# Kernel tuning notes

Hardware: AMD Instinct MI355X
Metric: run time of the kernel (lower is better)

The kernel has to match this reference:

```python
import jax, jax.numpy as jnp
import numpy as np

N, D_IN, D, K = 8192, 1024, 256, 30
SCALE = D ** (-0.5)


def setup_inputs() -> dict:
    key = jax.random.key(0)
    ks = jax.random.split(key, 10)
    p = lambda k, sh: (jax.random.normal(k, sh, dtype=jnp.float32) * 0.02)
    return {
        'x_path': jax.random.normal(ks[0], (N, D_IN), dtype=jnp.float32),
        'W_fc1': p(ks[1], (D_IN, D)), 'b_fc1': jnp.zeros((D,), jnp.float32),
        'W_fc2': p(ks[2], (D, D)),   'b_fc2': jnp.zeros((D,), jnp.float32),
        'W_head': p(ks[3], (D, D)),  'b_head': jnp.zeros((D,), jnp.float32),
        'W_tail': p(ks[4], (D, D)),  'b_tail': jnp.zeros((D,), jnp.float32),
        'W_lin1': p(ks[5], (D, D)),  'b_lin1': jnp.zeros((D,), jnp.float32),
        'W_lin2': p(ks[6], (D, D)),  'b_lin2': jnp.zeros((D,), jnp.float32),
        'W_att1': p(ks[7], (D, D // 2)), 'b_att1': jnp.zeros((D // 2,), jnp.float32),
        'W_att2': p(ks[8], (D // 2, 1)), 'b_att2': jnp.zeros((1,), jnp.float32),
    }


def reference(x_path, W_fc1, b_fc1, W_fc2, b_fc2, W_head, b_head, W_tail, b_tail,
              W_lin1, b_lin1, W_lin2, b_lin2, W_att1, b_att1, W_att2, b_att2):
    # pathology_fc (eval mode, dropout = identity): 1024 -> 256 -> 256
    h = jax.nn.relu(x_path @ W_fc1 + b_fc1)
    h = jax.nn.relu(h @ W_fc2 + b_fc2)                      # [N, D]

    e_h = h @ W_head + b_head                               # [N, D]
    e_t = h @ W_tail + b_tail                               # [N, D]

    # pairwise scores + topk neighbor selection
    attn_logit = (e_h * SCALE) @ e_t.T                      # [N, N]
    topk_w, topk_i = jax.lax.top_k(attn_logit, K)           # [N, K]
    topk_prob = jax.nn.softmax(topk_w, axis=-1)             # [N, K]

    Nb_h = e_t[topk_i]                                      # gather neighbors [N, K, D]

    # gated message construction
    eh_r = topk_prob[..., None] * Nb_h + (1.0 - topk_prob)[..., None] * e_h[:, None, :]
    gate = jnp.tanh(e_h[:, None, :] + eh_r)                 # [N, K, D]

    # torch.einsum('ijkl,ijkm->ijk', Nb_h, gate): l and m summed independently
    ka_weight = Nb_h.sum(-1) * gate.sum(-1)                 # [N, K]
    ka_prob = jax.nn.softmax(ka_weight, axis=-1)            # [N, K]
    e_Nh = jnp.einsum('nk,nkd->nd', ka_prob, Nb_h)          # [N, D]

    sum_emb = jax.nn.relu((e_h + e_Nh) @ W_lin1 + b_lin1)
    bi_emb = jax.nn.relu((e_h * e_Nh) @ W_lin2 + b_lin2)
    e = sum_emb + bi_emb                                    # [N, D]

    # GlobalAttention readout
    att = jax.nn.leaky_relu(e @ W_att1 + b_att1, 0.01) @ W_att2 + b_att2   # [N, 1]
    a = jax.nn.softmax(att, axis=0)                         # softmax over nodes
    e_g = (a * e).sum(0)                                    # [D]
    return e, e_g
```

## Files before the change

kernel.cpp:

```cpp
#include <hip/hip_runtime.h>
#include <math.h>

#define NN   8192
#define DIN  1024
#define DD   256
#define TOPK 30
#define KP   40
#define CAP  88
#define NINF -3e38f

typedef short s8v  __attribute__((ext_vector_type(8)));
typedef float f16v __attribute__((ext_vector_type(16)));

__device__ __forceinline__ float wred_sum(float v) {
  v += __shfl_down(v, 32); v += __shfl_down(v, 16); v += __shfl_down(v, 8);
  v += __shfl_down(v, 4);  v += __shfl_down(v, 2);  v += __shfl_down(v, 1);
  return v;
}
__device__ __forceinline__ float wred_max(float v) {
  v = fmaxf(v, __shfl_down(v, 32)); v = fmaxf(v, __shfl_down(v, 16));
  v = fmaxf(v, __shfl_down(v, 8));  v = fmaxf(v, __shfl_down(v, 4));
  v = fmaxf(v, __shfl_down(v, 2));  v = fmaxf(v, __shfl_down(v, 1));
  return v;
}
__device__ __forceinline__ float tanh_fast(float x) {
  return 1.f - 2.f / (__expf(2.f * x) + 1.f);
}
__device__ __forceinline__ unsigned short f2bf(float x) {
  union { float f; unsigned int u; } v; v.f = x;
  unsigned int r = v.u + 0x7FFF + ((v.u >> 16) & 1);
  return (unsigned short)(r >> 16);
}
__device__ __forceinline__ bool pair_gt(float v, int i, float pv, int pi) {
  return (v > pv) || (v == pv && i < pi);
}
__device__ __forceinline__ unsigned key_pack(float f, int col) {
  unsigned b = __float_as_uint(f);
  unsigned u = ((int)b < 0) ? ~b : (b | 0x80000000u);
  return (u & 0xFFFFE000u) | (unsigned)col;
}

template<int ACT, int AOP, int ACCUM>
__global__ __launch_bounds__(128, 4)
void gemm_k(const float* __restrict__ A, const float* __restrict__ A2,
            const float* __restrict__ B, const float* __restrict__ bias,
            float* __restrict__ C, int K, int NB)
{
  __shared__ float sA[32 * 36];
  __shared__ float sB[32 * 68];
  const int t  = threadIdx.x;
  const int rb = blockIdx.x * 32;
  const int cb = blockIdx.y * 64;
  const int tr = t >> 4;
  const int tc = t & 15;

  float acc[4][4];
#pragma unroll
  for (int u = 0; u < 4; ++u)
#pragma unroll
    for (int j = 0; j < 4; ++j) acc[u][j] = 0.f;

  const int sr  = t >> 2;
  const int sk2 = (t & 3) * 4;

  for (int kt = 0; kt < K; kt += 32) {
    __syncthreads();
    {
      const float* Ap = A + (size_t)(rb + sr) * K + kt;
      float4 va = *(const float4*)(Ap + sk2);
      float4 vb = *(const float4*)(Ap + sk2 + 16);
      if (AOP) {
        const float* A2p = A2 + (size_t)(rb + sr) * K + kt;
        const float4 wa = *(const float4*)(A2p + sk2);
        const float4 wb = *(const float4*)(A2p + sk2 + 16);
        if (AOP == 1) {
          va.x += wa.x; va.y += wa.y; va.z += wa.z; va.w += wa.w;
          vb.x += wb.x; vb.y += wb.y; vb.z += wb.z; vb.w += wb.w;
        } else {
          va.x *= wa.x; va.y *= wa.y; va.z *= wa.z; va.w *= wa.w;
          vb.x *= wb.x; vb.y *= wb.y; vb.z *= wb.z; vb.w *= wb.w;
        }
      }
      sA[(sk2 + 0) * 36 + sr] = va.x; sA[(sk2 + 1) * 36 + sr] = va.y;
      sA[(sk2 + 2) * 36 + sr] = va.z; sA[(sk2 + 3) * 36 + sr] = va.w;
      sA[(sk2 + 16) * 36 + sr] = vb.x; sA[(sk2 + 17) * 36 + sr] = vb.y;
      sA[(sk2 + 18) * 36 + sr] = vb.z; sA[(sk2 + 19) * 36 + sr] = vb.w;
    }
    {
#pragma unroll
      for (int i = 0; i < 4; ++i) {
        const int f4 = t + 128 * i;
        const int k  = f4 >> 4;
        const int c4 = (f4 & 15) << 2;
        *(float4*)&sB[k * 68 + c4] = *(const float4*)&B[(size_t)(kt + k) * NB + cb + c4];
      }
    }
    __syncthreads();
#pragma unroll 8
    for (int k = 0; k < 32; ++k) {
      const float4 bv = *(const float4*)&sB[k * 68 + 4 * tc];
      const float4 av = *(const float4*)&sA[k * 36 + 4 * tr];
      const float a[4] = {av.x, av.y, av.z, av.w};
      const float b[4] = {bv.x, bv.y, bv.z, bv.w};
#pragma unroll
      for (int u = 0; u < 4; ++u)
#pragma unroll
        for (int j = 0; j < 4; ++j) acc[u][j] = fmaf(a[u], b[j], acc[u][j]);
    }
  }

  const float4 bz = *(const float4*)&bias[cb + 4 * tc];
  const float bb[4] = {bz.x, bz.y, bz.z, bz.w};
#pragma unroll
  for (int u = 0; u < 4; ++u) {
    const int row = rb + 4 * tr + u;
    float o[4];
#pragma unroll
    for (int j = 0; j < 4; ++j) {
      o[j] = acc[u][j] + bb[j];
      if (ACT) o[j] = fmaxf(o[j], 0.f);
    }
    float* Cp = &C[(size_t)row * NB + cb + 4 * tc];
    if (ACCUM) {
      const float4 old = *(const float4*)Cp;
      o[0] += old.x; o[1] += old.y; o[2] += old.z; o[3] += old.w;
    }
    float4 ov; ov.x = o[0]; ov.y = o[1]; ov.z = o[2]; ov.w = o[3];
    *(float4*)Cp = ov;
  }
}

__global__ __launch_bounds__(256)
void pack_frag_k(const float* __restrict__ src, unsigned short* __restrict__ dst)
{
  const int c = blockIdx.x * 256 + threadIdx.x;
  const int l = c & 63;
  const int W = (c >> 6) & 15;
  const int T = c >> 10;
  const int col = T * 32 + (l & 31);
  const int k0  = W * 16 + ((l >> 5) << 3);
  const float4 a = *(const float4*)&src[(size_t)col * DD + k0];
  const float4 b = *(const float4*)&src[(size_t)col * DD + k0 + 4];
  uint4 o;
  o.x = (unsigned)f2bf(a.x) | ((unsigned)f2bf(a.y) << 16);
  o.y = (unsigned)f2bf(a.z) | ((unsigned)f2bf(a.w) << 16);
  o.z = (unsigned)f2bf(b.x) | ((unsigned)f2bf(b.y) << 16);
  o.w = (unsigned)f2bf(b.z) | ((unsigned)f2bf(b.w) << 16);
  *(uint4*)&dst[(size_t)c * 8] = o;
}

__global__ __launch_bounds__(256)
void rowsum_k(const float* __restrict__ et, float* __restrict__ rs)
{
  const int t = threadIdx.x, lane = t & 63, w = t >> 6;
  const int n = blockIdx.x * 4 + w;
  const float4 v = *(const float4*)&et[(size_t)n * DD + lane * 4];
  float s = v.x + v.y + v.z + v.w;
  s = wred_sum(s);
  if (lane == 0) rs[n] = s;
}

__global__ __launch_bounds__(512, 4)
void score_cand_k(const unsigned short* __restrict__ ehF,
                  const unsigned short* __restrict__ etF,
                  unsigned* __restrict__ gCand)
{
  __shared__ unsigned sBuf[32 * CAP];
  __shared__ unsigned sK[32][KP];
  __shared__ unsigned sThrK[32];
  __shared__ int      sCnt[32];

  const int t = threadIdx.x, lane = t & 63, w = t >> 6;
  const int g  = blockIdx.x;
  const int sy = blockIdx.y;
  const int tile0 = sy * 128;
  const s8v* eh8 = (const s8v*)ehF;
  const s8v* et8 = (const s8v*)etF;

  s8v af[16];
#pragma unroll
  for (int W = 0; W < 16; ++W)
    af[W] = eh8[((size_t)g * 16 + W) * 64 + lane];

  for (int idx = t; idx < 32 * KP; idx += 512) ((unsigned*)sK)[idx] = 0u;
  if (t < 32) { sThrK[t] = 0u; sCnt[t] = 0; }
  __syncthreads();

  const int rq = 4 * (lane >> 5);
  const int colLane = lane & 31;

  int tb = 0;
  for (int rnd = 0; rnd < 7; ++rnd) {
    const int ntile = (rnd == 0) ? 2 : (2 << (rnd - 1));
    for (int p = w; p < ntile; p += 8) {
      const int T = tile0 + tb + p;
      const s8v* bp = et8 + (size_t)T * 1024 + lane;
      f16v c;
#pragma unroll
      for (int i = 0; i < 16; ++i) c[i] = 0.f;
      {
        s8v b[8];
#pragma unroll
        for (int q = 0; q < 8; ++q) b[q] = bp[q * 64];
#pragma unroll
        for (int q = 0; q < 8; ++q)
          c = __builtin_amdgcn_mfma_f32_32x32x16_bf16(af[q], b[q], c, 0, 0, 0);
#pragma unroll
        for (int q = 0; q < 8; ++q) b[q] = bp[(8 + q) * 64];
#pragma unroll
        for (int q = 0; q < 8; ++q)
          c = __builtin_amdgcn_mfma_f32_32x32x16_bf16(af[8 + q], b[q], c, 0, 0, 0);
      }
      const int col = T * 32 + colLane;
#pragma unroll
      for (int r = 0; r < 16; ++r) {
        const int row = (r & 3) + 8 * (r >> 2) + rq;
        const unsigned key = key_pack(c[r], col);
        if (key > sThrK[row]) {
          const int ix = atomicAdd(&sCnt[row], 1);
          if (ix < CAP) sBuf[row * CAP + ix] = key;
        }
      }
    }
    __syncthreads();

#pragma unroll 1
    for (int rp = 0; rp < 2; ++rp) {
      const int ra = 4 * w + 2 * rp;
      const int rc = ra + 1;
      const int cA = min(sCnt[ra], CAP);
      const int cB = min(sCnt[rc], CAP);
      unsigned a0 = (lane < KP) ? sK[ra][lane]
                                : ((lane - KP) < cA ? sBuf[ra * CAP + (lane - KP)] : 0u);
      unsigned a1 = ((24 + lane) < cA) ? sBuf[ra * CAP + 24 + lane] : 0u;
      unsigned b0 = (lane < KP) ? sK[rc][lane]
                                : ((lane - KP) < cB ? sBuf[rc * CAP + (lane - KP)] : 0u);
      unsigned b1 = ((24 + lane) < cB) ? sBuf[rc * CAP + 24 + lane] : 0u;
#pragma unroll
      for (int k = 2; k <= 128; k <<= 1) {
#pragma unroll
        for (int j = k >> 1; j >= 1; j >>= 1) {
          if (j == 64) {
            unsigned mx = max(a0, a1), mn = min(a0, a1); a0 = mx; a1 = mn;
            mx = max(b0, b1); mn = min(b0, b1); b0 = mx; b1 = mn;
          } else {
            const unsigned pa0 = (unsigned)__shfl_xor((int)a0, j);
            const unsigned pa1 = (unsigned)__shfl_xor((int)a1, j);
            const unsigned pb0 = (unsigned)__shfl_xor((int)b0, j);
            const unsigned pb1 = (unsigned)__shfl_xor((int)b1, j);
            const bool km0 = (((lane & k) == 0)        == ((lane & j) == 0));
            const bool km1 = ((((64 + lane) & k) == 0) == ((lane & j) == 0));
            a0 = km0 ? max(a0, pa0) : min(a0, pa0);
            a1 = km1 ? max(a1, pa1) : min(a1, pa1);
            b0 = km0 ? max(b0, pb0) : min(b0, pb0);
            b1 = km1 ? max(b1, pb1) : min(b1, pb1);
          }
        }
      }
      if (rnd < 6) {
        if (lane < KP) { sK[ra][lane] = a0; sK[rc][lane] = b0; }
        if (lane == KP - 1) { sThrK[ra] = a0; sThrK[rc] = b0; }
        if (lane == 0) { sCnt[ra] = 0; sCnt[rc] = 0; }
      } else {
        if (lane < KP) {
          gCand[(((size_t)g * 2 + sy) * 32 + ra) * KP + lane] = a0;
          gCand[(((size_t)g * 2 + sy) * 32 + rc) * KP + lane] = b0;
        }
      }
    }
    __syncthreads();
    tb += ntile;
  }
}

__global__ __launch_bounds__(512, 2)
void cand_merge_k(const unsigned* __restrict__ gCand,
                  const float* __restrict__ e_h, const float* __restrict__ e_t,
                  float* __restrict__ topv_g, int* __restrict__ topi_g)
{
  __shared__ float    sEh[32 * 256];
  __shared__ unsigned sK40[32][KP];
  __shared__ float    sRes[32][KP];
  const int t = threadIdx.x, lane = t & 63, w = t >> 6;
  const int g = blockIdx.x, rb = g * 32;

  for (int i = t; i < 2048; i += 512)
    ((float4*)sEh)[i] = ((const float4*)(e_h + (size_t)rb * 256))[i];

#pragma unroll 1
  for (int rr = 0; rr < 4; ++rr) {
    const int r = 4 * w + rr;
    unsigned v0, v1;
    {
      const int m = lane;
      const int s = m / 40, q = m - s * 40;
      v0 = gCand[(((size_t)g * 2 + s) * 32 + r) * KP + q];
    }
    {
      const int m = 64 + lane;
      if (m < 80) {
        const int q = m - 40;
        v1 = gCand[(((size_t)g * 2 + 1) * 32 + r) * KP + q];
      } else v1 = 0u;
    }
#pragma unroll
    for (int k = 2; k <= 128; k <<= 1) {
#pragma unroll
      for (int j = k >> 1; j >= 1; j >>= 1) {
        if (j == 64) {
          const unsigned mx = max(v0, v1), mn = min(v0, v1);
          v0 = mx; v1 = mn;
        } else {
          const unsigned p0 = (unsigned)__shfl_xor((int)v0, j);
          const unsigned p1 = (unsigned)__shfl_xor((int)v1, j);
          const bool km0 = (((lane & k) == 0)        == ((lane & j) == 0));
          const bool km1 = ((((64 + lane) & k) == 0) == ((lane & j) == 0));
          v0 = km0 ? max(v0, p0) : min(v0, p0);
          v1 = km1 ? max(v1, p1) : min(v1, p1);
        }
      }
    }
    if (lane < KP) sK40[r][lane] = v0;
  }
  __syncthreads();

  for (int i = t; i < 32 * KP; i += 512) {
    const int r = i / KP, q = i - r * KP;
    const int c = (int)(sK40[r][q] & 0x1FFFu);
    const float* et = &e_t[(size_t)c * 256];
    const float* eh = &sEh[r * 256];
    float acc = 0.f;
#pragma unroll 8
    for (int d = 0; d < 64; ++d) {
      const float4 a = *(const float4*)&eh[d * 4];
      const float4 b = *(const float4*)&et[d * 4];
      acc = fmaf(a.x, b.x, acc); acc = fmaf(a.y, b.y, acc);
      acc = fmaf(a.z, b.z, acc); acc = fmaf(a.w, b.w, acc);
    }
    sRes[r][q] = acc * 0.0625f;
  }
  __syncthreads();

#pragma unroll 1
  for (int rr = 0; rr < 4; ++rr) {
    const int r = 4 * w + rr;
    float v; int c;
    if (lane < KP) { v = sRes[r][lane]; c = (int)(sK40[r][lane] & 0x1FFFu); }
    else           { v = NINF;          c = 0x40000000 + lane; }
#pragma unroll
    for (int k = 2; k <= 64; k <<= 1) {
#pragma unroll
      for (int j = k >> 1; j >= 1; j >>= 1) {
        const float pv = __shfl_xor(v, j);
        const int   pc = __shfl_xor(c, j);
        const bool km = (((lane & k) == 0) == ((lane & j) == 0));
        const bool gt = pair_gt(v, c, pv, pc);
        const bool keep = (km == gt);
        v = keep ? v : pv; c = keep ? c : pc;
      }
    }
    if (lane < TOPK) {
      topv_g[(size_t)(rb + r) * TOPK + lane] = v;
      topi_g[(size_t)(rb + r) * TOPK + lane] = c;
    }
  }
}

__global__ __launch_bounds__(256)
void message_k(const float* __restrict__ e_h, const float* __restrict__ e_t,
               const float* __restrict__ rs, const float* __restrict__ tv_g,
               const int* __restrict__ ti_g, float* __restrict__ e_Nh)
{
  __shared__ float sP[TOPK];
  __shared__ int   sI[TOPK];
  __shared__ float sW[TOPK];
  __shared__ float wpart[TOPK][4];
  const int n = blockIdx.x;
  const int t = threadIdx.x, lane = t & 63, w = t >> 6;

  if (w == 0) {
    const float v = (lane < TOPK) ? tv_g[(size_t)n * TOPK + lane] : NINF;
    float m = wred_max(v); m = __shfl(m, 0);
    const float p = (lane < TOPK) ? __expf(v - m) : 0.f;
    float s = wred_sum(p); s = __shfl(s, 0);
    if (lane < TOPK) { sP[lane] = p / s; sI[lane] = ti_g[(size_t)n * TOPK + lane]; }
  }
  __syncthreads();

  const float eh = e_h[(size_t)n * DD + t];
  float nbv[TOPK];
#pragma unroll
  for (int k = 0; k < TOPK; ++k) {
    const int   j = sI[k];
    const float p = sP[k];
    const float nb = e_t[(size_t)j * DD + t];
    nbv[k] = nb;
    float g = tanh_fast((2.f - p) * eh + p * nb);
    g = wred_sum(g);
    if (lane == 0) wpart[k][w] = g;
  }
  __syncthreads();

  if (w == 0) {
    float kw = NINF;
    if (lane < TOPK) {
      const float gs = wpart[lane][0] + wpart[lane][1] + wpart[lane][2] + wpart[lane][3];
      kw = rs[sI[lane]] * gs;
    }
    float m = wred_max(kw); m = __shfl(m, 0);
    const float p = (lane < TOPK) ? __expf(kw - m) : 0.f;
    float s = wred_sum(p); s = __shfl(s, 0);
    if (lane < TOPK) sW[lane] = p / s;
  }
  __syncthreads();

  float o = 0.f;
#pragma unroll
  for (int k = 0; k < TOPK; ++k) o = fmaf(sW[k], nbv[k], o);
  e_Nh[(size_t)n * DD + t] = o;
}

__global__ __launch_bounds__(256)
void att_k(const float* __restrict__ e, const float* __restrict__ W1,
           const float* __restrict__ b1, const float* __restrict__ W2,
           const float* __restrict__ b2, float* __restrict__ att)
{
  const int t = threadIdx.x;
  const int q = t >> 7;
  const int m = t & 127;
  const int lane = t & 63, w = t >> 6;
  const int n0 = blockIdx.x * 8 + q * 4;
  float acc[4] = {0.f, 0.f, 0.f, 0.f};
  for (int d = 0; d < DD; ++d) {
    const float wv = W1[d * 128 + m];
#pragma unroll
    for (int rr = 0; rr < 4; ++rr)
      acc[rr] = fmaf(e[(size_t)(n0 + rr) * DD + d], wv, acc[rr]);
  }
  const float b1m = b1[m], w2m = W2[m];
  __shared__ float part[4][4];
#pragma unroll
  for (int rr = 0; rr < 4; ++rr) {
    float v = acc[rr] + b1m;
    v = (v > 0.f) ? v : 0.01f * v;
    v *= w2m;
    v = wred_sum(v);
    if (lane == 0) part[w][rr] = v;
  }
  __syncthreads();
  if (t < 8) {
    const int qq = t >> 2, rr = t & 3;
    att[blockIdx.x * 8 + qq * 4 + rr] = part[qq * 2][rr] + part[qq * 2 + 1][rr] + b2[0];
  }
}

__global__ __launch_bounds__(1024)
void smax_prep_k(const float* __restrict__ att, float* __restrict__ stats,
                 float* __restrict__ eg)
{
  __shared__ float red[16];
  __shared__ float mg;
  const int t = threadIdx.x, lane = t & 63, w = t >> 6;
  float m = NINF;
#pragma unroll
  for (int i = 0; i < 8; ++i) m = fmaxf(m, att[t + 1024 * i]);
  m = wred_max(m);
  if (lane == 0) red[w] = m;
  __syncthreads();
  if (t == 0) {
    float mm = red[0];
    for (int i = 1; i < 16; ++i) mm = fmaxf(mm, red[i]);
    mg = mm;
  }
  __syncthreads();
  const float mm = mg;
  float s = 0.f;
#pragma unroll
  for (int i = 0; i < 8; ++i) s += __expf(att[t + 1024 * i] - mm);
  s = wred_sum(s);
  __syncthreads();
  if (lane == 0) red[w] = s;
  __syncthreads();
  if (t == 0) {
    float ss = 0.f;
    for (int i = 0; i < 16; ++i) ss += red[i];
    stats[0] = mm; stats[1] = ss;
  }
  if (t < DD) eg[t] = 0.f;
}

__global__ __launch_bounds__(256)
void eg_k(const float* __restrict__ att, const float* __restrict__ stats,
          const float* __restrict__ e, float* __restrict__ eg)
{
  const int t = threadIdx.x;
  const float m = stats[0], inv = 1.f / stats[1];
  float acc = 0.f;
  const int n0 = blockIdx.x * 128;
  for (int r = 0; r < 128; ++r) {
    const int n = n0 + r;
    acc = fmaf(__expf(att[n] - m), e[(size_t)n * DD + t], acc);
  }
  atomicAdd(&eg[t], acc * inv);
}

extern "C" void kernel_launch(void* const* d_in, const int* in_sizes, int n_in,
                              void* d_out, int out_size, void* d_ws, size_t ws_size,
                              hipStream_t stream)
{
  const float* x      = (const float*)d_in[0];
  const float* W_fc1  = (const float*)d_in[1];
  const float* b_fc1  = (const float*)d_in[2];
  const float* W_fc2  = (const float*)d_in[3];
  const float* b_fc2  = (const float*)d_in[4];
  const float* W_head = (const float*)d_in[5];
  const float* b_head = (const float*)d_in[6];
  const float* W_tail = (const float*)d_in[7];
  const float* b_tail = (const float*)d_in[8];
  const float* W_lin1 = (const float*)d_in[9];
  const float* b_lin1 = (const float*)d_in[10];
  const float* W_lin2 = (const float*)d_in[11];
  const float* b_lin2 = (const float*)d_in[12];
  const float* W_att1 = (const float*)d_in[13];
  const float* b_att1 = (const float*)d_in[14];
  const float* W_att2 = (const float*)d_in[15];
  const float* b_att2 = (const float*)d_in[16];

  float* out_e  = (float*)d_out;
  float* out_eg = out_e + (size_t)NN * DD;

  float* ws = (float*)d_ws;
  const size_t F = (size_t)NN * DD;
  float* e_h   = ws;
  float* e_t   = ws + F;
  float* e_Nh  = ws + 2 * F;
  float* bufA  = ws + 3 * F;
  float* bufB  = ws + 4 * F;
  float* rs    = ws + 5 * F;
  float* att   = rs + NN;
  float* stats = att + NN;
  float* topv  = stats + 16;
  int*   topi  = (int*)(topv + (size_t)NN * TOPK);

  unsigned short* ehF = (unsigned short*)bufA;
  unsigned short* etF = ehF + F;
  unsigned* gCand = (unsigned*)bufB;

  const dim3 blk(256);
  const dim3 gblk(128);
  const dim3 gemmGrid(NN / 32, DD / 64);

  gemm_k<1,0,0><<<gemmGrid, gblk, 0, stream>>>(x,    nullptr, W_fc1, b_fc1, bufA, DIN, DD);
  gemm_k<1,0,0><<<gemmGrid, gblk, 0, stream>>>(bufA, nullptr, W_fc2, b_fc2, bufB, DD,  DD);
  gemm_k<0,0,0><<<gemmGrid, gblk, 0, stream>>>(bufB, nullptr, W_head, b_head, e_h, DD, DD);
  gemm_k<0,0,0><<<gemmGrid, gblk, 0, stream>>>(bufB, nullptr, W_tail, b_tail, e_t, DD, DD);

  pack_frag_k<<<dim3(NN * DD / 8 / 256), blk, 0, stream>>>(e_h, ehF);
  pack_frag_k<<<dim3(NN * DD / 8 / 256), blk, 0, stream>>>(e_t, etF);
  rowsum_k<<<dim3(NN / 4), blk, 0, stream>>>(e_t, rs);

  score_cand_k<<<dim3(NN / 32, 2), dim3(512), 0, stream>>>(ehF, etF, gCand);
  cand_merge_k<<<dim3(NN / 32), dim3(512), 0, stream>>>(gCand, e_h, e_t, topv, topi);

  message_k<<<dim3(NN), blk, 0, stream>>>(e_h, e_t, rs, topv, topi, e_Nh);

  gemm_k<1,1,0><<<gemmGrid, gblk, 0, stream>>>(e_h, e_Nh, W_lin1, b_lin1, out_e, DD, DD);
  gemm_k<1,2,1><<<gemmGrid, gblk, 0, stream>>>(e_h, e_Nh, W_lin2, b_lin2, out_e, DD, DD);

  att_k<<<dim3(NN / 8), blk, 0, stream>>>(out_e, W_att1, b_att1, W_att2, b_att2, att);
  smax_prep_k<<<dim3(1), dim3(1024), 0, stream>>>(att, stats, out_eg);
  eg_k<<<dim3(64), blk, 0, stream>>>(att, stats, out_e, out_eg);
}
```

Measured before the change: 666.1 us.

## Aggregate candidate atomics per half-wave, split MFMA chains, and halve merge blocks

In the score kernel, each row's candidate insertions now use a ballot and popcount so that one atomicAdd runs per half-wave instead of one per passing lane. Per-row thresholds are cached in registers once per round rather than read from shared memory for every element. The 16-MFMA dependency chain is split into two independent accumulators to shorten the serial latency. The merge kernel now handles 16 rows per block across a 2-wide grid, doubling block count for better occupancy, at the cost of two extra sums per score and duplicate candidate loads.

```diff
diff --git a/kernel.cpp b/kernel.cpp
--- a/kernel.cpp
+++ b/kernel.cpp
@@ -188,36 +188,48 @@
 
   const int rq = 4 * (lane >> 5);
   const int colLane = lane & 31;
+  const int leader = (lane >> 5) << 5;
+  const unsigned lm = (1u << (lane & 31)) - 1;
 
   int tb = 0;
   for (int rnd = 0; rnd < 7; ++rnd) {
     const int ntile = (rnd == 0) ? 2 : (2 << (rnd - 1));
+    unsigned thrv[16];
+#pragma unroll
+    for (int r = 0; r < 16; ++r) thrv[r] = sThrK[(r & 3) + 8 * (r >> 2) + rq];
+
     for (int p = w; p < ntile; p += 8) {
       const int T = tile0 + tb + p;
       const s8v* bp = et8 + (size_t)T * 1024 + lane;
-      f16v c;
-#pragma unroll
-      for (int i = 0; i < 16; ++i) c[i] = 0.f;
+      f16v c0, c1;
+#pragma unroll
+      for (int i = 0; i < 16; ++i) { c0[i] = 0.f; c1[i] = 0.f; }
       {
         s8v b[8];
 #pragma unroll
         for (int q = 0; q < 8; ++q) b[q] = bp[q * 64];
 #pragma unroll
         for (int q = 0; q < 8; ++q)
-          c = __builtin_amdgcn_mfma_f32_32x32x16_bf16(af[q], b[q], c, 0, 0, 0);
+          c0 = __builtin_amdgcn_mfma_f32_32x32x16_bf16(af[q], b[q], c0, 0, 0, 0);
 #pragma unroll
         for (int q = 0; q < 8; ++q) b[q] = bp[(8 + q) * 64];
 #pragma unroll
         for (int q = 0; q < 8; ++q)
-          c = __builtin_amdgcn_mfma_f32_32x32x16_bf16(af[8 + q], b[q], c, 0, 0, 0);
+          c1 = __builtin_amdgcn_mfma_f32_32x32x16_bf16(af[8 + q], b[q], c1, 0, 0, 0);
       }
       const int col = T * 32 + colLane;
 #pragma unroll
       for (int r = 0; r < 16; ++r) {
         const int row = (r & 3) + 8 * (r >> 2) + rq;
-        const unsigned key = key_pack(c[r], col);
-        if (key > sThrK[row]) {
-          const int ix = atomicAdd(&sCnt[row], 1);
+        const unsigned key = key_pack(c0[r] + c1[r], col);
+        const bool pass = key > thrv[r];
+        const unsigned long long mask = __ballot(pass);
+        const unsigned hm = (unsigned)(mask >> leader);
+        int base = 0;
+        if ((lane & 31) == 0) base = atomicAdd(&sCnt[row], __popc(hm));
+        base = __shfl(base, leader);
+        if (pass) {
+          const int ix = base + __popc(hm & lm);
           if (ix < CAP) sBuf[row * CAP + ix] = key;
         }
       }
@@ -278,18 +290,20 @@
                   const float* __restrict__ e_h, const float* __restrict__ e_t,
                   float* __restrict__ topv_g, int* __restrict__ topi_g)
 {
-  __shared__ float    sEh[32 * 256];
-  __shared__ unsigned sK40[32][KP];
-  __shared__ float    sRes[32][KP];
+  __shared__ float    sEh[16 * 256];
+  __shared__ unsigned sK40[16][KP];
+  __shared__ float    sRes[16][KP];
   const int t = threadIdx.x, lane = t & 63, w = t >> 6;
   const int g = blockIdx.x, rb = g * 32;
-
-  for (int i = t; i < 2048; i += 512)
-    ((float4*)sEh)[i] = ((const float4*)(e_h + (size_t)rb * 256))[i];
+  const int r0 = blockIdx.y * 16;
+
+  for (int i = t; i < 1024; i += 512)
+    ((float4*)sEh)[i] = ((const float4*)(e_h + (size_t)(rb + r0) * 256))[i];
 
 #pragma unroll 1
-  for (int rr = 0; rr < 4; ++rr) {
-    const int r = 4 * w + rr;
+  for (int rp = 0; rp < 2; ++rp) {
+    const int lr = 2 * w + rp;
+    const int r  = r0 + lr;
     unsigned v0, v1;
     {
       const int m = lane;
@@ -320,15 +334,15 @@
         }
       }
     }
-    if (lane < KP) sK40[r][lane] = v0;
-  }
-  __syncthreads();
-
-  for (int i = t; i < 32 * KP; i += 512) {
-    const int r = i / KP, q = i - r * KP;
-    const int c = (int)(sK40[r][q] & 0x1FFFu);
+    if (lane < KP) sK40[lr][lane] = v0;
+  }
+  __syncthreads();
+
+  for (int i = t; i < 16 * KP; i += 512) {
+    const int lr = i / KP, q = i - lr * KP;
+    const int c = (int)(sK40[lr][q] & 0x1FFFu);
     const float* et = &e_t[(size_t)c * 256];
-    const float* eh = &sEh[r * 256];
+    const float* eh = &sEh[lr * 256];
     float acc = 0.f;
 #pragma unroll 8
     for (int d = 0; d < 64; ++d) {
@@ -337,16 +351,16 @@
       acc = fmaf(a.x, b.x, acc); acc = fmaf(a.y, b.y, acc);
       acc = fmaf(a.z, b.z, acc); acc = fmaf(a.w, b.w, acc);
     }
-    sRes[r][q] = acc * 0.0625f;
+    sRes[lr][q] = acc * 0.0625f;
   }
   __syncthreads();
 
 #pragma unroll 1
-  for (int rr = 0; rr < 4; ++rr) {
-    const int r = 4 * w + rr;
+  for (int rp = 0; rp < 2; ++rp) {
+    const int lr = 2 * w + rp;
     float v; int c;
-    if (lane < KP) { v = sRes[r][lane]; c = (int)(sK40[r][lane] & 0x1FFFu); }
-    else           { v = NINF;          c = 0x40000000 + lane; }
+    if (lane < KP) { v = sRes[lr][lane]; c = (int)(sK40[lr][lane] & 0x1FFFu); }
+    else           { v = NINF;           c = 0x40000000 + lane; }
 #pragma unroll
     for (int k = 2; k <= 64; k <<= 1) {
 #pragma unroll
@@ -360,8 +374,8 @@
       }
     }
     if (lane < TOPK) {
-      topv_g[(size_t)(rb + r) * TOPK + lane] = v;
-      topi_g[(size_t)(rb + r) * TOPK + lane] = c;
+      topv_g[(size_t)(rb + r0 + lr) * TOPK + lane] = v;
+      topi_g[(size_t)(rb + r0 + lr) * TOPK + lane] = c;
     }
   }
 }
@@ -560,7 +574,7 @@
   rowsum_k<<<dim3(NN / 4), blk, 0, stream>>>(e_t, rs);
 
   score_cand_k<<<dim3(NN / 32, 2), dim3(512), 0, stream>>>(ehF, etF, gCand);
-  cand_merge_k<<<dim3(NN / 32), dim3(512), 0, stream>>>(gCand, e_h, e_t, topv, topi);
+  cand_merge_k<<<dim3(NN / 32, 2), dim3(512), 0, stream>>>(gCand, e_h, e_t, topv, topi);
 
   message_k<<<dim3(NN), blk, 0, stream>>>(e_h, e_t, rs, topv, topi, e_Nh);
 
```

Result: slower. 727.4 us (+9.2%).
